# Kernel tuning notes

Measured on AMD Instinct MI355X. Metric: run time of the kernel, lower is better.

## Reference

```python
import jax, jax.numpy as jnp
import numpy as np

N, C = 262144, 128

def setup_inputs() -> dict:
    key = jax.random.key(0)
    k1, k2 = jax.random.split(key)
    x = jax.random.normal(k1, (N, C), dtype=jnp.float32)
    # binary label matrix (0/1 floats), as implied by the _target[i][0]==0 check
    target = jax.random.randint(k2, (N, C), 0, 2).astype(jnp.float32)
    return {"x": x, "target": target}

def reference(x, target):
    # Per-row argmax over classes (torch.max(_input[i], 0) -> idx)
    idx = jnp.argmax(x, axis=1)                      # [N]
    # Rows where idx > 0 and target[i,0] == 0 get all non-idx target entries zeroed
    cond = (idx > 0) & (target[:, 0] == 0)           # [N]
    keep = jax.nn.one_hot(idx, x.shape[1], dtype=target.dtype)  # [N, C]
    t = jnp.where(cond[:, None], target * keep, target)
    return jnp.mean(jnp.abs(x * t))
```

## Files before the change

kernel.cpp:

```cpp
#include <hip/hip_runtime.h>
#include <math.h>

#define NROWS 262144
#define NCOLS 128
#define TPB 256
#define NBLOCKS (NROWS / TPB)

__global__ __launch_bounds__(TPB) void biased_loss_rows(
    const float* __restrict__ x, const float* __restrict__ t,
    float* __restrict__ partial)
{
    const int row = blockIdx.x * TPB + threadIdx.x;
    const float4* xr = (const float4*)(x + (size_t)row * NCOLS);
    const float4* tr = (const float4*)(t + (size_t)row * NCOLS);

    float acc0 = 0.f, acc1 = 0.f;
    float bv = -INFINITY; int bi = 0; float bc = 0.f;
    float t0 = 0.f;

    #pragma unroll
    for (int j = 0; j < NCOLS / 4; ++j) {
        const float4 xv = xr[j];
        const float4 tv = tr[j];
        if (j == 0) t0 = tv.x;

        const float c0 = fabsf(xv.x * tv.x);
        const float c1 = fabsf(xv.y * tv.y);
        const float c2 = fabsf(xv.z * tv.z);
        const float c3 = fabsf(xv.w * tv.w);
        acc0 += c0 + c1;
        acc1 += c2 + c3;

        const bool s01 = xv.y > xv.x;
        const float v01 = s01 ? xv.y : xv.x;
        const int   i01 = 4 * j + (s01 ? 1 : 0);
        const float w01 = s01 ? c1 : c0;

        const bool s23 = xv.w > xv.z;
        const float v23 = s23 ? xv.w : xv.z;
        const int   i23 = 4 * j + 2 + (s23 ? 1 : 0);
        const float w23 = s23 ? c3 : c2;

        const bool sm = v23 > v01;
        const float vm = sm ? v23 : v01;
        const int   im = sm ? i23 : i01;
        const float wm = sm ? w23 : w01;

        const bool sb = vm > bv;
        bv = sb ? vm : bv;
        bi = sb ? im : bi;
        bc = sb ? wm : bc;
    }

    const bool cond = (bi > 0) && (t0 == 0.0f);
    float rowsum = cond ? bc : (acc0 + acc1);

    #pragma unroll
    for (int off = 32; off > 0; off >>= 1)
        rowsum += __shfl_xor(rowsum, off, 64);

    __shared__ float smem[TPB / 64];
    const int lane = threadIdx.x & 63, w = threadIdx.x >> 6;
    if (lane == 0) smem[w] = rowsum;
    __syncthreads();
    if (threadIdx.x == 0) {
        float b = 0.f;
        #pragma unroll
        for (int i = 0; i < TPB / 64; ++i) b += smem[i];
        partial[blockIdx.x] = b;
    }
}

__global__ __launch_bounds__(256) void reduce_partials(
    const float* __restrict__ partial, float* __restrict__ out, int n)
{
    float acc = 0.0f;
    for (int i = threadIdx.x; i < n; i += 256) acc += partial[i];
    #pragma unroll
    for (int off = 32; off > 0; off >>= 1)
        acc += __shfl_xor(acc, off, 64);
    __shared__ float smem[4];
    const int lane = threadIdx.x & 63, w = threadIdx.x >> 6;
    if (lane == 0) smem[w] = acc;
    __syncthreads();
    if (threadIdx.x == 0) {
        float s = smem[0] + smem[1] + smem[2] + smem[3];
        out[0] = s / (float)((size_t)NROWS * (size_t)NCOLS);
    }
}

extern "C" void kernel_launch(void* const* d_in, const int* in_sizes, int n_in,
                              void* d_out, int out_size, void* d_ws, size_t ws_size,
                              hipStream_t stream) {
    const float* x = (const float*)d_in[0];
    const float* t = (const float*)d_in[1];
    float* partial = (float*)d_ws;

    biased_loss_rows<<<NBLOCKS, TPB, 0, stream>>>(x, t, partial);
    reduce_partials<<<1, 256, 0, stream>>>(partial, (float*)d_out, NBLOCKS);
}
```

Measured before the change: 286.9 us.

## Stage 64-row tiles into LDS via direct global-to-LDS loads, split rows across threads

Replaces the one-thread-per-row scheme, whose per-thread strided float4 loads coalesce poorly. Each block now copies a contiguous 64-row tile of x and target into shared memory with global_load_lds 16-byte DMA. Four threads then process each row, using a rotated column order to avoid LDS bank conflicts. Partial argmax and sum results are merged through shared memory, breaking ties toward the first index. In exchange, the 64KB of LDS per block limits occupancy, and nothing overlaps loading with compute.

```diff
diff --git a/kernel.cpp b/kernel.cpp
--- a/kernel.cpp
+++ b/kernel.cpp
@@ -1,73 +1,100 @@
 #include <hip/hip_runtime.h>
 #include <math.h>
+#include <stdint.h>
 
 #define NROWS 262144
 #define NCOLS 128
+#define TILE_ROWS 64
 #define TPB 256
-#define NBLOCKS (NROWS / TPB)
+#define NTILES (NROWS / TILE_ROWS)
+#define TILE_FLOATS (TILE_ROWS * NCOLS)
+#define TILE_F4 (TILE_FLOATS / 4)
+#define F4_PER_THREAD (TILE_F4 / TPB)
 
-__global__ __launch_bounds__(TPB) void biased_loss_rows(
+__device__ __forceinline__ void dma16(const float* g, const float* l)
+{
+    __builtin_amdgcn_global_load_lds(
+        (__attribute__((address_space(1))) void*)(uintptr_t)g,
+        (__attribute__((address_space(3))) void*)(uint32_t)(uintptr_t)l,
+        16, 0, 0);
+}
+
+__global__ __launch_bounds__(TPB) void biased_loss_tile(
     const float* __restrict__ x, const float* __restrict__ t,
     float* __restrict__ partial)
 {
-    const int row = blockIdx.x * TPB + threadIdx.x;
-    const float4* xr = (const float4*)(x + (size_t)row * NCOLS);
-    const float4* tr = (const float4*)(t + (size_t)row * NCOLS);
+    __shared__ float smem[2 * TILE_FLOATS];
+    float* xs = smem;
+    float* ts = smem + TILE_FLOATS;
 
-    float acc0 = 0.f, acc1 = 0.f;
-    float bv = -INFINITY; int bi = 0; float bc = 0.f;
-    float t0 = 0.f;
+    const int tid  = threadIdx.x;
+    const int tile = blockIdx.x;
+    const float* gx = x + (size_t)tile * TILE_FLOATS;
+    const float* gt = t + (size_t)tile * TILE_FLOATS;
 
     #pragma unroll
-    for (int j = 0; j < NCOLS / 4; ++j) {
-        const float4 xv = xr[j];
-        const float4 tv = tr[j];
-        if (j == 0) t0 = tv.x;
+    for (int i = 0; i < F4_PER_THREAD; ++i) {
+        const int f4 = i * TPB + tid;
+        dma16(gx + 4 * f4, xs + 4 * f4);
+    }
+    #pragma unroll
+    for (int i = 0; i < F4_PER_THREAD; ++i) {
+        const int f4 = i * TPB + tid;
+        dma16(gt + 4 * f4, ts + 4 * f4);
+    }
+    __syncthreads();
 
-        const float c0 = fabsf(xv.x * tv.x);
-        const float c1 = fabsf(xv.y * tv.y);
-        const float c2 = fabsf(xv.z * tv.z);
-        const float c3 = fabsf(xv.w * tv.w);
-        acc0 += c0 + c1;
-        acc1 += c2 + c3;
+    const int r = tid & 63;
+    const int q = tid >> 6;
+    const int rot = r & 31;
+    const float* xrow = xs + r * NCOLS + q * 32;
 
-        const bool s01 = xv.y > xv.x;
-        const float v01 = s01 ? xv.y : xv.x;
-        const int   i01 = 4 * j + (s01 ? 1 : 0);
-        const float w01 = s01 ? c1 : c0;
-
-        const bool s23 = xv.w > xv.z;
-        const float v23 = s23 ? xv.w : xv.z;
-        const int   i23 = 4 * j + 2 + (s23 ? 1 : 0);
-        const float w23 = s23 ? c3 : c2;
-
-        const bool sm = v23 > v01;
-        const float vm = sm ? v23 : v01;
-        const int   im = sm ? i23 : i01;
-        const float wm = sm ? w23 : w01;
-
-        const bool sb = vm > bv;
-        bv = sb ? vm : bv;
-        bi = sb ? im : bi;
-        bc = sb ? wm : bc;
+    float bv = -INFINITY; int bi = 0x7fffffff; float bc = 0.f; float ps = 0.f;
+    #pragma unroll
+    for (int j = 0; j < 32; ++j) {
+        const int c = (j + rot) & 31;
+        const float xv = xrow[c];
+        const float tv = xrow[c + TILE_FLOATS];
+        const float p  = fabsf(xv * tv);
+        ps += p;
+        const int idx = q * 32 + c;
+        const bool take = (xv > bv) || (xv == bv && idx < bi);
+        bv = take ? xv : bv;
+        bi = take ? idx : bi;
+        bc = take ? p  : bc;
     }
 
-    const bool cond = (bi > 0) && (t0 == 0.0f);
-    float rowsum = cond ? bc : (acc0 + acc1);
+    __syncthreads();
 
-    #pragma unroll
-    for (int off = 32; off > 0; off >>= 1)
-        rowsum += __shfl_xor(rowsum, off, 64);
+    float* sv = smem;
+    int*   si = (int*)(smem + 256);
+    float* sc = smem + 512;
+    float* ss = smem + 768;
+    sv[tid] = bv; si[tid] = bi; sc[tid] = bc; ss[tid] = ps;
+    __syncthreads();
 
-    __shared__ float smem[TPB / 64];
-    const int lane = threadIdx.x & 63, w = threadIdx.x >> 6;
-    if (lane == 0) smem[w] = rowsum;
-    __syncthreads();
-    if (threadIdx.x == 0) {
-        float b = 0.f;
+    if (tid < 64) {
+        float mbv = sv[tid]; int mbi = si[tid]; float mbc = sc[tid];
+        float sum = ss[tid];
         #pragma unroll
-        for (int i = 0; i < TPB / 64; ++i) b += smem[i];
-        partial[blockIdx.x] = b;
+        for (int qq = 1; qq < 4; ++qq) {
+            const float ov = sv[qq * 64 + tid];
+            const int   oi = si[qq * 64 + tid];
+            const float oc = sc[qq * 64 + tid];
+            sum += ss[qq * 64 + tid];
+            const bool take = (ov > mbv) || (ov == mbv && oi < mbi);
+            mbv = take ? ov : mbv;
+            mbi = take ? oi : mbi;
+            mbc = take ? oc : mbc;
+        }
+        const float t0 = ts[tid * NCOLS];
+        const bool cond = (mbi > 0) && (t0 == 0.0f);
+        float acc = cond ? mbc : sum;
+
+        #pragma unroll
+        for (int off = 32; off > 0; off >>= 1)
+            acc += __shfl_xor(acc, off, 64);
+        if (tid == 0) partial[tile] = acc;
     }
 }
 
@@ -96,6 +123,6 @@
     const float* t = (const float*)d_in[1];
     float* partial = (float*)d_ws;
 
-    biased_loss_rows<<<NBLOCKS, TPB, 0, stream>>>(x, t, partial);
-    reduce_partials<<<1, 256, 0, stream>>>(partial, (float*)d_out, NBLOCKS);
+    biased_loss_tile<<<NTILES, TPB, 0, stream>>>(x, t, partial);
+    reduce_partials<<<1, 256, 0, stream>>>(partial, (float*)d_out, NTILES);
 }
```

Result: faster. 276.5 us (-3.6%).
